# Performance work log

Hardware: AMD Instinct MI355X
Metric: run time of the kernel (lower is better)

The kernel has to match this reference:

```python
import jax, jax.numpy as jnp
import numpy as np

B, IN, H = 4096, 1024, 1024


def setup_inputs() -> dict:
    key = jax.random.key(0)
    ks = jax.random.split(key, 16)
    s = 1.0 / np.sqrt(IN)
    inp = {
        "x_t": jax.random.normal(ks[0], (B, IN), jnp.float32),
        "h_prev": jax.random.normal(ks[1], (B, H), jnp.float32),
        "c_prev": jax.random.normal(ks[2], (B, H), jnp.float32),
        "W_xi": jax.random.uniform(ks[3], (H, IN), jnp.float32, -s, s),
        "W_hi": jax.random.normal(ks[4], (H, H), jnp.float32) / np.sqrt(H),
        "b_i": jnp.zeros((H,), jnp.float32),
        "W_xf": jax.random.uniform(ks[5], (H, IN), jnp.float32, -s, s),
        "W_hf": jax.random.normal(ks[6], (H, H), jnp.float32) / np.sqrt(H),
        "b_f": jnp.ones((H,), jnp.float32),
        "W_xg": jax.random.uniform(ks[7], (H, IN), jnp.float32, -s, s),
        "W_hg": jax.random.normal(ks[8], (H, H), jnp.float32) / np.sqrt(H),
        "b_g": jnp.zeros((H,), jnp.float32),
        "W_xo": jax.random.uniform(ks[9], (H, IN), jnp.float32, -s, s),
        "W_ho": jax.random.normal(ks[10], (H, H), jnp.float32) / np.sqrt(H),
        "b_o": jnp.zeros((H,), jnp.float32),
    }
    return inp


def reference(x_t, h_prev, c_prev,
              W_xi, W_hi, b_i,
              W_xf, W_hf, b_f,
              W_xg, W_hg, b_g,
              W_xo, W_ho, b_o):
    # i/f/g/o gates: sigmoid/sigmoid/tanh/sigmoid of (x W_x^T + h W_h^T + b)
    i_t = jax.nn.sigmoid(x_t @ W_xi.T + h_prev @ W_hi.T + b_i)
    f_t = jax.nn.sigmoid(x_t @ W_xf.T + h_prev @ W_hf.T + b_f)
    g_t = jnp.tanh(x_t @ W_xg.T + h_prev @ W_hg.T + b_g)
    o_t = jax.nn.sigmoid(x_t @ W_xo.T + h_prev @ W_ho.T + b_o)
    c_t = f_t * c_prev + i_t * g_t
    h_t = o_t * jnp.tanh(c_t)
    return (h_t, c_t)
```

## Files before the change

### kernel.cpp

```cpp
#include <hip/hip_runtime.h>
#include <hip/hip_bf16.h>


constexpr int Mdim = 4096;
constexpr int Ndim = 4096;
constexpr int Kdim = 2048;
constexpr int Hdim = 1024;
constexpr int BM = 128;
constexpr int BN = 256;
constexpr int BK = 64;
constexpr int NT = Kdim / BK;

using short8 = __attribute__((ext_vector_type(8))) short;
using f32x4  = __attribute__((ext_vector_type(4))) float;

__device__ __forceinline__ float sigmoid_(float x) {
    return 1.f / (1.f + __expf(-x));
}
__device__ __forceinline__ float tanh_(float x) {
    float e = __expf(2.f * x);
    return (e - 1.f) / (e + 1.f);
}

__global__ void build_A(const float* __restrict__ x, const float* __restrict__ h,
                        __hip_bfloat16* __restrict__ A) {
    int idx = blockIdx.x * 256 + threadIdx.x;
    int row = idx >> 8;
    int c8  = (idx & 255) * 8;
    const float* src = (c8 < 1024) ? (x + (size_t)row * 1024 + c8)
                                   : (h + (size_t)row * 1024 + (c8 - 1024));
    float4 f0 = ((const float4*)src)[0];
    float4 f1 = ((const float4*)src)[1];
    union { short8 v; __hip_bfloat16 e[8]; } u;
    u.e[0] = __float2bfloat16(f0.x); u.e[1] = __float2bfloat16(f0.y);
    u.e[2] = __float2bfloat16(f0.z); u.e[3] = __float2bfloat16(f0.w);
    u.e[4] = __float2bfloat16(f1.x); u.e[5] = __float2bfloat16(f1.y);
    u.e[6] = __float2bfloat16(f1.z); u.e[7] = __float2bfloat16(f1.w);
    *(short8*)(A + (size_t)row * Kdim + c8) = u.v;
}

__global__ void build_B(const float* __restrict__ Wxi, const float* __restrict__ Whi,
                        const float* __restrict__ Wxf, const float* __restrict__ Whf,
                        const float* __restrict__ Wxg, const float* __restrict__ Whg,
                        const float* __restrict__ Wxo, const float* __restrict__ Who,
                        __hip_bfloat16* __restrict__ B) {
    int idx = blockIdx.x * 256 + threadIdx.x;
    int n  = idx >> 8;
    int c8 = (idx & 255) * 8;
    int g = (n >> 4) & 3;
    int j = ((n >> 6) << 4) | (n & 15);
    const float* Wx = (g == 0) ? Wxi : (g == 1) ? Wxf : (g == 2) ? Wxg : Wxo;
    const float* Wh = (g == 0) ? Whi : (g == 1) ? Whf : (g == 2) ? Whg : Who;
    const float* src = (c8 < 1024) ? (Wx + (size_t)j * 1024 + c8)
                                   : (Wh + (size_t)j * 1024 + (c8 - 1024));
    float4 f0 = ((const float4*)src)[0];
    float4 f1 = ((const float4*)src)[1];
    union { short8 v; __hip_bfloat16 e[8]; } u;
    u.e[0] = __float2bfloat16(f0.x); u.e[1] = __float2bfloat16(f0.y);
    u.e[2] = __float2bfloat16(f0.z); u.e[3] = __float2bfloat16(f0.w);
    u.e[4] = __float2bfloat16(f1.x); u.e[5] = __float2bfloat16(f1.y);
    u.e[6] = __float2bfloat16(f1.z); u.e[7] = __float2bfloat16(f1.w);
    *(short8*)(B + (size_t)n * Kdim + c8) = u.v;
}

#define RD(p) (*(const short8*)(p))

__launch_bounds__(512, 4)
__global__ void lstm_gemm(const __hip_bfloat16* __restrict__ A,
                          const __hip_bfloat16* __restrict__ B,
                          const float* __restrict__ c_prev,
                          const float* __restrict__ b_i, const float* __restrict__ b_f,
                          const float* __restrict__ b_g, const float* __restrict__ b_o,
                          float* __restrict__ out_h, float* __restrict__ out_c) {
    __shared__ __hip_bfloat16 As[128 * 64];
    __shared__ __hip_bfloat16 Bs[256 * 64];

    const int tid  = threadIdx.x;
    const int lane = tid & 63;
    const int w    = tid >> 6;
    const int wr   = w >> 2;
    const int wc   = w & 3;
    const int l15  = lane & 15, lhi = lane >> 4;

    int bid = blockIdx.x;
    int swz = (bid & 7) * 64 + (bid >> 3);
    const int bm = (swz >> 4) * BM;
    const int bn = (swz & 15) * BN;

    const int srow_  = tid >> 3;
    const int schunk = ((tid & 7) ^ ((tid >> 3) & 7)) * 8;

    const int swz4 = (l15 & 7) << 4;

#define STG1(dstbase, byteoff, srcptr, grow, kcol)                              \
    __builtin_amdgcn_global_load_lds(                                           \
        (const __attribute__((address_space(1))) unsigned*)(                    \
            (srcptr) + (size_t)((grow) + srow_) * Kdim + (kcol) + schunk),      \
        (__attribute__((address_space(3))) unsigned*)(                          \
            (char*)(dstbase) + (byteoff) + tid * 16), 16, 0, 0)

#define STAGE_TILE(kc)                                                          \
    do {                                                                        \
        STG1(As, 0,     A, bm + 0,   kc);                                       \
        STG1(As, 8192,  A, bm + 64,  kc);                                       \
        STG1(Bs, 0,     B, bn + 0,   kc);                                       \
        STG1(Bs, 8192,  B, bn + 64,  kc);                                       \
        STG1(Bs, 16384, B, bn + 128, kc);                                       \
        STG1(Bs, 24576, B, bn + 192, kc);                                       \
    } while (0)

    f32x4 acc[4][4];
#pragma unroll
    for (int a = 0; a < 4; ++a)
#pragma unroll
        for (int b = 0; b < 4; ++b)
            acc[a][b] = (f32x4){0.f, 0.f, 0.f, 0.f};

    STAGE_TILE(0);
    __builtin_amdgcn_sched_barrier(0);
    asm volatile("s_waitcnt vmcnt(0)" ::: "memory");
    __builtin_amdgcn_s_barrier();

    for (int t = 0; t < NT; ++t) {
#pragma unroll
        for (int kk = 0; kk < 2; ++kk) {
            const int kof = (kk * 64 + lhi * 16) ^ swz4;
            short8 af[4], bf[4];
#pragma unroll
            for (int a = 0; a < 4; ++a)
                af[a] = RD((const char*)As + (wr * 64 + a * 16 + l15) * 128 + kof);
#pragma unroll
            for (int b = 0; b < 4; ++b)
                bf[b] = RD((const char*)Bs + (wc * 64 + b * 16 + l15) * 128 + kof);
            __builtin_amdgcn_s_setprio(1);
#pragma unroll
            for (int a = 0; a < 4; ++a)
#pragma unroll
                for (int b = 0; b < 4; ++b)
                    acc[a][b] = __builtin_amdgcn_mfma_f32_16x16x32_bf16(
                        af[a], bf[b], acc[a][b], 0, 0, 0);
            __builtin_amdgcn_s_setprio(0);
        }

        if (t + 1 < NT) {
            __builtin_amdgcn_s_barrier();
            STAGE_TILE((t + 1) * BK);
            __builtin_amdgcn_sched_barrier(0);
            asm volatile("s_waitcnt vmcnt(0)" ::: "memory");
            __builtin_amdgcn_s_barrier();
        }
    }
#undef STG1
#undef STAGE_TILE

    const int j0 = ((bn + wc * 64) >> 6) * 16 + l15;
    const float bi  = b_i[j0];
    const float bf_ = b_f[j0];
    const float bg  = b_g[j0];
    const float bo  = b_o[j0];

#pragma unroll
    for (int a = 0; a < 4; ++a) {
        int mbase = bm + wr * 64 + a * 16 + lhi * 4;
#pragma unroll
        for (int r = 0; r < 4; ++r) {
            int m = mbase + r;
            float vi = acc[a][0][r] + bi;
            float vf = acc[a][1][r] + bf_;
            float vg = acc[a][2][r] + bg;
            float vo = acc[a][3][r] + bo;
            float it = sigmoid_(vi);
            float ft = sigmoid_(vf);
            float gt = tanh_(vg);
            float ot = sigmoid_(vo);
            float cp = c_prev[(size_t)m * Hdim + j0];
            float ct = ft * cp + it * gt;
            float ht = ot * tanh_(ct);
            out_h[(size_t)m * Hdim + j0] = ht;
            out_c[(size_t)m * Hdim + j0] = ct;
        }
    }
}

extern "C" void kernel_launch(void* const* d_in, const int* in_sizes, int n_in,
                              void* d_out, int out_size, void* d_ws, size_t ws_size,
                              hipStream_t stream) {
    const float* x_t    = (const float*)d_in[0];
    const float* h_prev = (const float*)d_in[1];
    const float* c_prev = (const float*)d_in[2];
    const float* W_xi   = (const float*)d_in[3];
    const float* W_hi   = (const float*)d_in[4];
    const float* b_i    = (const float*)d_in[5];
    const float* W_xf   = (const float*)d_in[6];
    const float* W_hf   = (const float*)d_in[7];
    const float* b_f    = (const float*)d_in[8];
    const float* W_xg   = (const float*)d_in[9];
    const float* W_hg   = (const float*)d_in[10];
    const float* b_g    = (const float*)d_in[11];
    const float* W_xo   = (const float*)d_in[12];
    const float* W_ho   = (const float*)d_in[13];
    const float* b_o    = (const float*)d_in[14];

    float* out_h = (float*)d_out;
    float* out_c = out_h + (size_t)Mdim * Hdim;

    __hip_bfloat16* Abf = (__hip_bfloat16*)d_ws;
    __hip_bfloat16* Bbf = Abf + (size_t)Mdim * Kdim;

    build_A<<<4096, 256, 0, stream>>>(x_t, h_prev, Abf);
    build_B<<<4096, 256, 0, stream>>>(W_xi, W_hi, W_xf, W_hf, W_xg, W_hg, W_xo, W_ho, Bbf);

    lstm_gemm<<<dim3((Mdim / BM) * (Ndim / BN)), 512, 0, stream>>>(
        Abf, Bbf, c_prev, b_i, b_f, b_g, b_o, out_h, out_c);
}
```

Measured before the change: 87.20 us.

## Triple-buffer GEMM K tiles with BK=32 prefetch and merge conversion kernels

The GEMM main loop now uses three LDS stages with a K tile of 32, issuing global-to-LDS loads two tiles ahead. Partial vmcnt waits let loads overlap MFMA work instead of draining memory on every tile. The LDS layout and XOR swizzle are reworked for the smaller tile. The separate A and B bf16 conversion kernels are merged into one launch to save launch overhead. The cost is twice as many barriers per K step and more intricate wait-count bookkeeping.

Result: slower. 93.74 us (+7.5%).

```diff
diff --git a/kernel.cpp b/kernel.cpp
--- a/kernel.cpp
+++ b/kernel.cpp
@@ -8,7 +8,7 @@
 constexpr int Hdim = 1024;
 constexpr int BM = 128;
 constexpr int BN = 256;
-constexpr int BK = 64;
+constexpr int BK = 32;
 constexpr int NT = Kdim / BK;
 
 using short8 = __attribute__((ext_vector_type(8))) short;
@@ -22,13 +22,31 @@
     return (e - 1.f) / (e + 1.f);
 }
 
-__global__ void build_A(const float* __restrict__ x, const float* __restrict__ h,
-                        __hip_bfloat16* __restrict__ A) {
-    int idx = blockIdx.x * 256 + threadIdx.x;
+__global__ void build_AB(const float* __restrict__ x, const float* __restrict__ h,
+                         const float* __restrict__ Wxi, const float* __restrict__ Whi,
+                         const float* __restrict__ Wxf, const float* __restrict__ Whf,
+                         const float* __restrict__ Wxg, const float* __restrict__ Whg,
+                         const float* __restrict__ Wxo, const float* __restrict__ Who,
+                         __hip_bfloat16* __restrict__ A, __hip_bfloat16* __restrict__ B) {
+    int bidx = blockIdx.x;
+    const float* src;
+    __hip_bfloat16* dst;
+    int idx = (bidx & 4095) * 256 + threadIdx.x;
     int row = idx >> 8;
     int c8  = (idx & 255) * 8;
-    const float* src = (c8 < 1024) ? (x + (size_t)row * 1024 + c8)
-                                   : (h + (size_t)row * 1024 + (c8 - 1024));
+    if (bidx < 4096) {
+        src = (c8 < 1024) ? (x + (size_t)row * 1024 + c8)
+                          : (h + (size_t)row * 1024 + (c8 - 1024));
+        dst = A + (size_t)row * Kdim + c8;
+    } else {
+        int g = (row >> 4) & 3;
+        int j = ((row >> 6) << 4) | (row & 15);
+        const float* Wx = (g == 0) ? Wxi : (g == 1) ? Wxf : (g == 2) ? Wxg : Wxo;
+        const float* Wh = (g == 0) ? Whi : (g == 1) ? Whf : (g == 2) ? Whg : Who;
+        src = (c8 < 1024) ? (Wx + (size_t)j * 1024 + c8)
+                          : (Wh + (size_t)j * 1024 + (c8 - 1024));
+        dst = B + (size_t)row * Kdim + c8;
+    }
     float4 f0 = ((const float4*)src)[0];
     float4 f1 = ((const float4*)src)[1];
     union { short8 v; __hip_bfloat16 e[8]; } u;
@@ -36,31 +54,7 @@
     u.e[2] = __float2bfloat16(f0.z); u.e[3] = __float2bfloat16(f0.w);
     u.e[4] = __float2bfloat16(f1.x); u.e[5] = __float2bfloat16(f1.y);
     u.e[6] = __float2bfloat16(f1.z); u.e[7] = __float2bfloat16(f1.w);
-    *(short8*)(A + (size_t)row * Kdim + c8) = u.v;
-}
-
-__global__ void build_B(const float* __restrict__ Wxi, const float* __restrict__ Whi,
-                        const float* __restrict__ Wxf, const float* __restrict__ Whf,
-                        const float* __restrict__ Wxg, const float* __restrict__ Whg,
-                        const float* __restrict__ Wxo, const float* __restrict__ Who,
-                        __hip_bfloat16* __restrict__ B) {
-    int idx = blockIdx.x * 256 + threadIdx.x;
-    int n  = idx >> 8;
-    int c8 = (idx & 255) * 8;
-    int g = (n >> 4) & 3;
-    int j = ((n >> 6) << 4) | (n & 15);
-    const float* Wx = (g == 0) ? Wxi : (g == 1) ? Wxf : (g == 2) ? Wxg : Wxo;
-    const float* Wh = (g == 0) ? Whi : (g == 1) ? Whf : (g == 2) ? Whg : Who;
-    const float* src = (c8 < 1024) ? (Wx + (size_t)j * 1024 + c8)
-                                   : (Wh + (size_t)j * 1024 + (c8 - 1024));
-    float4 f0 = ((const float4*)src)[0];
-    float4 f1 = ((const float4*)src)[1];
-    union { short8 v; __hip_bfloat16 e[8]; } u;
-    u.e[0] = __float2bfloat16(f0.x); u.e[1] = __float2bfloat16(f0.y);
-    u.e[2] = __float2bfloat16(f0.z); u.e[3] = __float2bfloat16(f0.w);
-    u.e[4] = __float2bfloat16(f1.x); u.e[5] = __float2bfloat16(f1.y);
-    u.e[6] = __float2bfloat16(f1.z); u.e[7] = __float2bfloat16(f1.w);
-    *(short8*)(B + (size_t)n * Kdim + c8) = u.v;
+    *(short8*)dst = u.v;
 }
 
 #define RD(p) (*(const short8*)(p))
@@ -72,8 +66,7 @@
                           const float* __restrict__ b_i, const float* __restrict__ b_f,
                           const float* __restrict__ b_g, const float* __restrict__ b_o,
                           float* __restrict__ out_h, float* __restrict__ out_c) {
-    __shared__ __hip_bfloat16 As[128 * 64];
-    __shared__ __hip_bfloat16 Bs[256 * 64];
+    __shared__ __hip_bfloat16 lds[3][3][128 * 32];
 
     const int tid  = threadIdx.x;
     const int lane = tid & 63;
@@ -87,26 +80,25 @@
     const int bm = (swz >> 4) * BM;
     const int bn = (swz & 15) * BN;
 
-    const int srow_  = tid >> 3;
-    const int schunk = ((tid & 7) ^ ((tid >> 3) & 7)) * 8;
-
-    const int swz4 = (l15 & 7) << 4;
-
-#define STG1(dstbase, byteoff, srcptr, grow, kcol)                              \
+    const int srow_  = tid >> 2;
+    const int schunk = ((tid & 3) ^ ((tid >> 3) & 3)) * 8;
+
+    const int koff = ((lhi ^ ((l15 >> 1) & 3)) << 4);
+    const int offA = (wr * 64 + l15) * 64 + koff;
+    const int offB = (wc >> 1) * 8192 + ((wc & 1) * 64 + l15) * 64 + koff;
+
+#define STG1(dstbase, srcptr, grow, kcol)                                       \
     __builtin_amdgcn_global_load_lds(                                           \
         (const __attribute__((address_space(1))) unsigned*)(                    \
             (srcptr) + (size_t)((grow) + srow_) * Kdim + (kcol) + schunk),      \
         (__attribute__((address_space(3))) unsigned*)(                          \
-            (char*)(dstbase) + (byteoff) + tid * 16), 16, 0, 0)
-
-#define STAGE_TILE(kc)                                                          \
+            (char*)(dstbase) + tid * 16), 16, 0, 0)
+
+#define STAGE_TILE(s, kc)                                                       \
     do {                                                                        \
-        STG1(As, 0,     A, bm + 0,   kc);                                       \
-        STG1(As, 8192,  A, bm + 64,  kc);                                       \
-        STG1(Bs, 0,     B, bn + 0,   kc);                                       \
-        STG1(Bs, 8192,  B, bn + 64,  kc);                                       \
-        STG1(Bs, 16384, B, bn + 128, kc);                                       \
-        STG1(Bs, 24576, B, bn + 192, kc);                                       \
+        STG1(&lds[s][0][0], A, bm + 0,   kc);                                   \
+        STG1(&lds[s][1][0], B, bn + 0,   kc);                                   \
+        STG1(&lds[s][2][0], B, bn + 128, kc);                                   \
     } while (0)
 
     f32x4 acc[4][4];
@@ -116,42 +108,48 @@
         for (int b = 0; b < 4; ++b)
             acc[a][b] = (f32x4){0.f, 0.f, 0.f, 0.f};
 
-    STAGE_TILE(0);
-    __builtin_amdgcn_sched_barrier(0);
-    asm volatile("s_waitcnt vmcnt(0)" ::: "memory");
+    STAGE_TILE(0, 0);
+    STAGE_TILE(1, BK);
+    asm volatile("s_waitcnt vmcnt(3)" ::: "memory");
     __builtin_amdgcn_s_barrier();
 
-    for (int t = 0; t < NT; ++t) {
-#pragma unroll
-        for (int kk = 0; kk < 2; ++kk) {
-            const int kof = (kk * 64 + lhi * 16) ^ swz4;
-            short8 af[4], bf[4];
-#pragma unroll
-            for (int a = 0; a < 4; ++a)
-                af[a] = RD((const char*)As + (wr * 64 + a * 16 + l15) * 128 + kof);
-#pragma unroll
-            for (int b = 0; b < 4; ++b)
-                bf[b] = RD((const char*)Bs + (wc * 64 + b * 16 + l15) * 128 + kof);
-            __builtin_amdgcn_s_setprio(1);
-#pragma unroll
-            for (int a = 0; a < 4; ++a)
-#pragma unroll
-                for (int b = 0; b < 4; ++b)
-                    acc[a][b] = __builtin_amdgcn_mfma_f32_16x16x32_bf16(
-                        af[a], bf[b], acc[a][b], 0, 0, 0);
-            __builtin_amdgcn_s_setprio(0);
-        }
-
-        if (t + 1 < NT) {
-            __builtin_amdgcn_s_barrier();
-            STAGE_TILE((t + 1) * BK);
-            __builtin_amdgcn_sched_barrier(0);
-            asm volatile("s_waitcnt vmcnt(0)" ::: "memory");
-            __builtin_amdgcn_s_barrier();
-        }
+#define BODY(t_, sR_, sW_)                                                      \
+    do {                                                                        \
+        if ((t_) + 2 < NT) STAGE_TILE(sW_, ((t_) + 2) * BK);                    \
+        const char* Ab = (const char*)&lds[sR_][0][0] + offA;                   \
+        const char* Bb = (const char*)&lds[sR_][1][0] + offB;                   \
+        short8 af[4], bf[4];                                                    \
+        _Pragma("unroll")                                                       \
+        for (int a = 0; a < 4; ++a) af[a] = RD(Ab + a * 1024);                  \
+        _Pragma("unroll")                                                       \
+        for (int b = 0; b < 4; ++b) bf[b] = RD(Bb + b * 1024);                  \
+        __builtin_amdgcn_s_setprio(1);                                          \
+        _Pragma("unroll")                                                       \
+        for (int a = 0; a < 4; ++a)                                             \
+            _Pragma("unroll")                                                   \
+            for (int b = 0; b < 4; ++b)                                         \
+                acc[a][b] = __builtin_amdgcn_mfma_f32_16x16x32_bf16(            \
+                    af[a], bf[b], acc[a][b], 0, 0, 0);                          \
+        __builtin_amdgcn_s_setprio(0);                                          \
+        if ((t_) + 1 < NT) {                                                    \
+            __builtin_amdgcn_sched_barrier(0);                                  \
+            if ((t_) + 2 < NT)                                                  \
+                asm volatile("s_waitcnt vmcnt(3) lgkmcnt(0)" ::: "memory");     \
+            else                                                                \
+                asm volatile("s_waitcnt vmcnt(0) lgkmcnt(0)" ::: "memory");     \
+            __builtin_amdgcn_s_barrier();                                       \
+        }                                                                       \
+    } while (0)
+
+    for (int t3 = 0; t3 < NT - 1; t3 += 3) {
+        BODY(t3 + 0, 0, 2);
+        BODY(t3 + 1, 1, 0);
+        BODY(t3 + 2, 2, 1);
     }
+    BODY(NT - 1, 0, 2);
 #undef STG1
 #undef STAGE_TILE
+#undef BODY
 
     const int j0 = ((bn + wc * 64) >> 6) * 16 + l15;
     const float bi  = b_i[j0];
@@ -207,8 +205,8 @@
     __hip_bfloat16* Abf = (__hip_bfloat16*)d_ws;
     __hip_bfloat16* Bbf = Abf + (size_t)Mdim * Kdim;
 
-    build_A<<<4096, 256, 0, stream>>>(x_t, h_prev, Abf);
-    build_B<<<4096, 256, 0, stream>>>(W_xi, W_hi, W_xf, W_hf, W_xg, W_hg, W_xo, W_ho, Bbf);
+    build_AB<<<8192, 256, 0, stream>>>(x_t, h_prev, W_xi, W_hi, W_xf, W_hf,
+                                       W_xg, W_hg, W_xo, W_ho, Abf, Bbf);
 
     lstm_gemm<<<dim3((Mdim / BM) * (Ndim / BN)), 512, 0, stream>>>(
         Abf, Bbf, c_prev, b_i, b_f, b_g, b_o, out_h, out_c);
```

## Merge bf16 conversion kernels and shrink GEMM tile to 128x128 with 4 waves

Applied to the files above, without the earlier changes.

Combines the two fp32-to-bf16 packing kernels into one launch, removing a kernel launch and its tail. The GEMM block tile shrinks from 128x256 with 8 waves to 128x128 with 4 waves. That doubles the grid to 1024 blocks for better CU balance and cuts LDS per block. The block-swizzle mapping and staging offsets are updated to match. Each wave still computes a 64x64 subtile, but the smaller tile means less reuse of staged A data across the N dimension.

Result: slower. 92.51 us (+6.1%).

```diff
diff --git a/kernel.cpp b/kernel.cpp
--- a/kernel.cpp
+++ b/kernel.cpp
@@ -7,7 +7,7 @@
 constexpr int Kdim = 2048;
 constexpr int Hdim = 1024;
 constexpr int BM = 128;
-constexpr int BN = 256;
+constexpr int BN = 128;
 constexpr int BK = 64;
 constexpr int NT = Kdim / BK;
 
@@ -22,13 +22,31 @@
     return (e - 1.f) / (e + 1.f);
 }
 
-__global__ void build_A(const float* __restrict__ x, const float* __restrict__ h,
-                        __hip_bfloat16* __restrict__ A) {
-    int idx = blockIdx.x * 256 + threadIdx.x;
+__global__ void build_AB(const float* __restrict__ x, const float* __restrict__ h,
+                         const float* __restrict__ Wxi, const float* __restrict__ Whi,
+                         const float* __restrict__ Wxf, const float* __restrict__ Whf,
+                         const float* __restrict__ Wxg, const float* __restrict__ Whg,
+                         const float* __restrict__ Wxo, const float* __restrict__ Who,
+                         __hip_bfloat16* __restrict__ A, __hip_bfloat16* __restrict__ B) {
+    int bidx = blockIdx.x;
+    const float* src;
+    __hip_bfloat16* dst;
+    int idx = (bidx & 4095) * 256 + threadIdx.x;
     int row = idx >> 8;
     int c8  = (idx & 255) * 8;
-    const float* src = (c8 < 1024) ? (x + (size_t)row * 1024 + c8)
-                                   : (h + (size_t)row * 1024 + (c8 - 1024));
+    if (bidx < 4096) {
+        src = (c8 < 1024) ? (x + (size_t)row * 1024 + c8)
+                          : (h + (size_t)row * 1024 + (c8 - 1024));
+        dst = A + (size_t)row * Kdim + c8;
+    } else {
+        int g = (row >> 4) & 3;
+        int j = ((row >> 6) << 4) | (row & 15);
+        const float* Wx = (g == 0) ? Wxi : (g == 1) ? Wxf : (g == 2) ? Wxg : Wxo;
+        const float* Wh = (g == 0) ? Whi : (g == 1) ? Whf : (g == 2) ? Whg : Who;
+        src = (c8 < 1024) ? (Wx + (size_t)j * 1024 + c8)
+                          : (Wh + (size_t)j * 1024 + (c8 - 1024));
+        dst = B + (size_t)row * Kdim + c8;
+    }
     float4 f0 = ((const float4*)src)[0];
     float4 f1 = ((const float4*)src)[1];
     union { short8 v; __hip_bfloat16 e[8]; } u;
@@ -36,36 +54,12 @@
     u.e[2] = __float2bfloat16(f0.z); u.e[3] = __float2bfloat16(f0.w);
     u.e[4] = __float2bfloat16(f1.x); u.e[5] = __float2bfloat16(f1.y);
     u.e[6] = __float2bfloat16(f1.z); u.e[7] = __float2bfloat16(f1.w);
-    *(short8*)(A + (size_t)row * Kdim + c8) = u.v;
-}
-
-__global__ void build_B(const float* __restrict__ Wxi, const float* __restrict__ Whi,
-                        const float* __restrict__ Wxf, const float* __restrict__ Whf,
-                        const float* __restrict__ Wxg, const float* __restrict__ Whg,
-                        const float* __restrict__ Wxo, const float* __restrict__ Who,
-                        __hip_bfloat16* __restrict__ B) {
-    int idx = blockIdx.x * 256 + threadIdx.x;
-    int n  = idx >> 8;
-    int c8 = (idx & 255) * 8;
-    int g = (n >> 4) & 3;
-    int j = ((n >> 6) << 4) | (n & 15);
-    const float* Wx = (g == 0) ? Wxi : (g == 1) ? Wxf : (g == 2) ? Wxg : Wxo;
-    const float* Wh = (g == 0) ? Whi : (g == 1) ? Whf : (g == 2) ? Whg : Who;
-    const float* src = (c8 < 1024) ? (Wx + (size_t)j * 1024 + c8)
-                                   : (Wh + (size_t)j * 1024 + (c8 - 1024));
-    float4 f0 = ((const float4*)src)[0];
-    float4 f1 = ((const float4*)src)[1];
-    union { short8 v; __hip_bfloat16 e[8]; } u;
-    u.e[0] = __float2bfloat16(f0.x); u.e[1] = __float2bfloat16(f0.y);
-    u.e[2] = __float2bfloat16(f0.z); u.e[3] = __float2bfloat16(f0.w);
-    u.e[4] = __float2bfloat16(f1.x); u.e[5] = __float2bfloat16(f1.y);
-    u.e[6] = __float2bfloat16(f1.z); u.e[7] = __float2bfloat16(f1.w);
-    *(short8*)(B + (size_t)n * Kdim + c8) = u.v;
+    *(short8*)dst = u.v;
 }
 
 #define RD(p) (*(const short8*)(p))
 
-__launch_bounds__(512, 4)
+__launch_bounds__(256, 4)
 __global__ void lstm_gemm(const __hip_bfloat16* __restrict__ A,
                           const __hip_bfloat16* __restrict__ B,
                           const float* __restrict__ c_prev,
@@ -73,19 +67,19 @@
                           const float* __restrict__ b_g, const float* __restrict__ b_o,
                           float* __restrict__ out_h, float* __restrict__ out_c) {
     __shared__ __hip_bfloat16 As[128 * 64];
-    __shared__ __hip_bfloat16 Bs[256 * 64];
+    __shared__ __hip_bfloat16 Bs[128 * 64];
 
     const int tid  = threadIdx.x;
     const int lane = tid & 63;
     const int w    = tid >> 6;
-    const int wr   = w >> 2;
-    const int wc   = w & 3;
+    const int wr   = w >> 1;
+    const int wc   = w & 1;
     const int l15  = lane & 15, lhi = lane >> 4;
 
     int bid = blockIdx.x;
-    int swz = (bid & 7) * 64 + (bid >> 3);
-    const int bm = (swz >> 4) * BM;
-    const int bn = (swz & 15) * BN;
+    int swz = (bid & 7) * 128 + (bid >> 3);
+    const int bm = (swz >> 5) * BM;
+    const int bn = (swz & 31) * BN;
 
     const int srow_  = tid >> 3;
     const int schunk = ((tid & 7) ^ ((tid >> 3) & 7)) * 8;
@@ -101,12 +95,14 @@
 
 #define STAGE_TILE(kc)                                                          \
     do {                                                                        \
-        STG1(As, 0,     A, bm + 0,   kc);                                       \
-        STG1(As, 8192,  A, bm + 64,  kc);                                       \
-        STG1(Bs, 0,     B, bn + 0,   kc);                                       \
-        STG1(Bs, 8192,  B, bn + 64,  kc);                                       \
-        STG1(Bs, 16384, B, bn + 128, kc);                                       \
-        STG1(Bs, 24576, B, bn + 192, kc);                                       \
+        STG1(As, 0,     A, bm + 0,  kc);                                        \
+        STG1(As, 4096,  A, bm + 32, kc);                                        \
+        STG1(As, 8192,  A, bm + 64, kc);                                        \
+        STG1(As, 12288, A, bm + 96, kc);                                        \
+        STG1(Bs, 0,     B, bn + 0,  kc);                                        \
+        STG1(Bs, 4096,  B, bn + 32, kc);                                        \
+        STG1(Bs, 8192,  B, bn + 64, kc);                                        \
+        STG1(Bs, 12288, B, bn + 96, kc);                                        \
     } while (0)
 
     f32x4 acc[4][4];
@@ -207,9 +203,9 @@
     __hip_bfloat16* Abf = (__hip_bfloat16*)d_ws;
     __hip_bfloat16* Bbf = Abf + (size_t)Mdim * Kdim;
 
-    build_A<<<4096, 256, 0, stream>>>(x_t, h_prev, Abf);
-    build_B<<<4096, 256, 0, stream>>>(W_xi, W_hi, W_xf, W_hf, W_xg, W_hg, W_xo, W_ho, Bbf);
-
-    lstm_gemm<<<dim3((Mdim / BM) * (Ndim / BN)), 512, 0, stream>>>(
+    build_AB<<<8192, 256, 0, stream>>>(x_t, h_prev, W_xi, W_hi, W_xf, W_hf,
+                                       W_xg, W_hg, W_xo, W_ho, Abf, Bbf);
+
+    lstm_gemm<<<dim3((Mdim / BM) * (Ndim / BN)), 256, 0, stream>>>(
         Abf, Bbf, c_prev, b_i, b_f, b_g, b_o, out_h, out_c);
 }
```
